# Kernel optimization log

Measured on AMD Instinct MI355X. Metric: run time of the kernel, lower is better.

Reference implementation:

```python
import jax, jax.numpy as jnp
import numpy as np

HIDDEN = 2048
HEADS = 16
HEAD_DIM = HIDDEN // HEADS
B, L = 4, 2048


def _rotate_half(x):
    x1, x2 = jnp.split(x, 2, axis=-1)
    return jnp.concatenate([-x2, x1], axis=-1)


def setup_inputs() -> dict:
    key = jax.random.key(0)
    k1, k2, k3 = jax.random.split(key, 3)
    x = jax.random.normal(k1, (B, L, HIDDEN), dtype=jnp.float32)
    # realistic rotary tables
    inv_freq = 1.0 / (10000.0 ** (jnp.arange(0, HEAD_DIM, 2, dtype=jnp.float32) / HEAD_DIM))
    t = jnp.arange(L, dtype=jnp.float32)
    freqs = jnp.outer(t, inv_freq)  # [L, HEAD_DIM/2]
    emb = jnp.concatenate([freqs, freqs], axis=-1)  # [L, HEAD_DIM]
    cos = jnp.cos(emb)
    sin = jnp.sin(emb)
    w_qkv = jax.random.normal(k2, (3 * HIDDEN, HIDDEN), dtype=jnp.float32) * (HIDDEN ** -0.5)
    w_out = jax.random.normal(k3, (HIDDEN, HIDDEN), dtype=jnp.float32) * (HIDDEN ** -0.5)
    return {"x": x, "cos": cos, "sin": sin, "w_qkv": w_qkv, "w_out": w_out}


def reference(x, cos, sin, w_qkv, w_out):
    b, l, d = x.shape
    qkv = jnp.einsum('bld,ed->ble', x, w_qkv)  # [B, L, 3D]
    q, k, v = jnp.split(qkv, 3, axis=-1)
    # [B, H, L, Dh]
    q = q.reshape(b, l, HEADS, HEAD_DIM).transpose(0, 2, 1, 3)
    k = k.reshape(b, l, HEADS, HEAD_DIM).transpose(0, 2, 1, 3)
    v = v.reshape(b, l, HEADS, HEAD_DIM).transpose(0, 2, 1, 3)
    cos_ = cos[None, None, :l, :]
    sin_ = sin[None, None, :l, :]
    q = q * cos_ + _rotate_half(q) * sin_
    k = k * cos_ + _rotate_half(k) * sin_
    scale = 1.0 / jnp.sqrt(jnp.asarray(HEAD_DIM, dtype=q.dtype))
    scores = jnp.einsum('bhqd,bhkd->bhqk', q, k) * scale
    attn = jax.nn.softmax(scores, axis=-1)
    out = jnp.einsum('bhqk,bhkd->bhqd', attn, v)  # [B, H, L, Dh]
    out = out.transpose(0, 2, 1, 3).reshape(b, l, d)
    return jnp.einsum('bld,ed->ble', out, w_out)
```

## Files before the change

### kernel.cpp

```cpp
#include <hip/hip_runtime.h>
#include <cstdint>
#include <cstddef>

typedef unsigned short u16;
typedef __attribute__((ext_vector_type(8))) short bf16x8;
typedef __attribute__((ext_vector_type(4))) float f32x4;

#define DEVFN static __device__ __forceinline__

DEVFN u16 f2bf(float f) {
  unsigned u = __float_as_uint(f);
  unsigned r = (u + 0x7FFFu + ((u >> 16) & 1u)) >> 16;
  return (u16)r;
}

DEVFN void gload16(const void* g, void* l) {
  __builtin_amdgcn_global_load_lds(
      (const __attribute__((address_space(1))) void*)g,
      (__attribute__((address_space(3))) void*)l, 16, 0, 0);
}

#define WAITVM(n) asm volatile("s_waitcnt vmcnt(" #n ")" ::: "memory")
#define BARRIER() do { asm volatile("" ::: "memory"); \
                       __builtin_amdgcn_s_barrier();   \
                       asm volatile("" ::: "memory"); } while (0)
#define FENCE_LDS() do { asm volatile("s_waitcnt lgkmcnt(0)" ::: "memory"); \
                         __builtin_amdgcn_sched_barrier(0); } while (0)

__global__ void prep(const float* __restrict__ x, const float* __restrict__ wqkv,
                     const float* __restrict__ wout, const float* __restrict__ cosp,
                     const float* __restrict__ sinp, u16* __restrict__ xb,
                     u16* __restrict__ wqkvb, u16* __restrict__ woutb,
                     float2* __restrict__ cs) {
  constexpr int X4 = 4194304;
  constexpr int W4 = 3145728;
  constexpr int O4 = 1048576;
  int i = blockIdx.x * blockDim.x + threadIdx.x;
  if (i < X4) {
    float4 v = ((const float4*)x)[i];
    unsigned long long w = (unsigned long long)f2bf(v.x)
        | ((unsigned long long)f2bf(v.y) << 16)
        | ((unsigned long long)f2bf(v.z) << 32)
        | ((unsigned long long)f2bf(v.w) << 48);
    *(unsigned long long*)(xb + (size_t)i * 4) = w;
  } else if (i < X4 + W4) {
    int j = i - X4;
    int base = j * 4;
    int e = base >> 11, col = base & 2047;
    int e2;
    if (e < 4096) {
      int part = e >> 11, loc = e & 2047;
      int h = loc >> 7, d = loc & 127;
      int d2 = (d < 64) ? 2 * d : 2 * (d - 64) + 1;
      e2 = part * 2048 + h * 128 + d2;
    } else {
      e2 = e;
    }
    float4 v = *(const float4*)&wqkv[(size_t)base];
    unsigned long long w = (unsigned long long)f2bf(v.x)
        | ((unsigned long long)f2bf(v.y) << 16)
        | ((unsigned long long)f2bf(v.z) << 32)
        | ((unsigned long long)f2bf(v.w) << 48);
    *(unsigned long long*)(wqkvb + (size_t)e2 * 2048 + col) = w;
  } else if (i < X4 + W4 + O4) {
    int j = i - X4 - W4;
    float4 v = ((const float4*)wout)[j];
    unsigned long long w = (unsigned long long)f2bf(v.x)
        | ((unsigned long long)f2bf(v.y) << 16)
        | ((unsigned long long)f2bf(v.z) << 32)
        | ((unsigned long long)f2bf(v.w) << 48);
    *(unsigned long long*)(woutb + (size_t)j * 4) = w;
  } else {
    int k = i - X4 - W4 - O4;
    int ld4 = k * 4;
#pragma unroll
    for (int u = 0; u < 4; u++) {
      int ld = ld4 + u;
      int l = ld >> 6, d = ld & 63;
      cs[ld] = make_float2(cosp[(size_t)l * 128 + d], sinp[(size_t)l * 128 + d]);
    }
  }
}

enum { M_F32OUT = 0, M_ROPE = 1, M_VT = 2 };

DEVFN bf16x8 rdfrag(const u16* buf, int row, int chunk) {
  return *(const bf16x8*)&buf[row * 64 + (((chunk ^ (row & 7)) & 7) << 3)];
}

template <int MODE, int Q>
DEVFN void phase_mfma(const u16* Ac, const u16* Bc, int wm, int wn, int quad, int l16,
                      bf16x8 (&bfr)[4][2], f32x4 (&acc)[8][4]) {
  if (Q == 0) {
#pragma unroll
    for (int j = 0; j < 4; j++)
#pragma unroll
      for (int kk = 0; kk < 2; kk++)
        bfr[j][kk] = rdfrag(Bc, wn * 64 + j * 16 + l16, kk * 4 + quad);
  }
  bf16x8 af[2][2];
#pragma unroll
  for (int i2 = 0; i2 < 2; i2++)
#pragma unroll
    for (int kk = 0; kk < 2; kk++)
      af[i2][kk] = rdfrag(Ac, wm * 128 + (Q * 2 + i2) * 16 + l16, kk * 4 + quad);
  __builtin_amdgcn_s_setprio(1);
#pragma unroll
  for (int kk = 0; kk < 2; kk++)
#pragma unroll
    for (int i2 = 0; i2 < 2; i2++)
#pragma unroll
      for (int j = 0; j < 4; j++) {
        if (MODE == M_VT)
          acc[Q * 2 + i2][j] = __builtin_amdgcn_mfma_f32_16x16x32_bf16(
              bfr[j][kk], af[i2][kk], acc[Q * 2 + i2][j], 0, 0, 0);
        else
          acc[Q * 2 + i2][j] = __builtin_amdgcn_mfma_f32_16x16x32_bf16(
              af[i2][kk], bfr[j][kk], acc[Q * 2 + i2][j], 0, 0, 0);
      }
  __builtin_amdgcn_s_setprio(0);
}

template <int MODE>
DEVFN void gemm256_core(const u16* __restrict__ A, const u16* __restrict__ Bt,
                        void* __restrict__ Cv, const float2* __restrict__ cs,
                        int N, int m0, int n0, u16* As, u16* Bs) {
  int tid = threadIdx.x;
  int wv = tid >> 6, lane = tid & 63, quad = lane >> 4, l16 = lane & 15;
  int wm = wv >> 2, wn = wv & 3;

  const u16* pB[2][2];
  const u16* pA[4];
#pragma unroll
  for (int h = 0; h < 2; h++)
#pragma unroll
    for (int o = 0; o < 2; o++) {
      int r = h * 128 + o * 64 + wv * 8 + (lane >> 3);
      int ck = (lane & 7) ^ (r & 7);
      pB[h][o] = Bt + (size_t)(n0 + r) * 2048 + ck * 8;
    }
#pragma unroll
  for (int q = 0; q < 4; q++) {
    int rb = (wv < 4) ? (q * 32 + wv * 8) : (128 + q * 32 + (wv - 4) * 8);
    int r = rb + (lane >> 3);
    int ck = (lane & 7) ^ (r & 7);
    pA[q] = A + (size_t)(m0 + r) * 2048 + ck * 8;
  }

#define STAGE_B(h, buf, kk) do {                                    \
    int rb0_ = (h) * 128 + wv * 8;                                  \
    gload16(pB[h][0] + (kk), &(buf)[rb0_ * 64]);                    \
    gload16(pB[h][1] + (kk), &(buf)[(rb0_ + 64) * 64]); } while (0)
#define STAGE_A(q, buf, kk) do {                                    \
    int rb_ = ((wv < 4) ? ((q) * 32 + wv * 8)                       \
                        : (128 + (q) * 32 + (wv - 4) * 8));         \
    gload16(pA[q] + (kk), &(buf)[rb_ * 64]); } while (0)

  f32x4 acc[8][4] = {};
  bf16x8 bfr[4][2];

  STAGE_B(0, Bs, 0);
  STAGE_B(1, Bs, 0);
  STAGE_A(0, As, 0);
  STAGE_A(1, As, 0);
  STAGE_A(2, As, 0);
  STAGE_A(3, As, 0);

  for (int t = 0; t < 31; t++) {
    const u16* Ac = As + (t & 1) * 16384;
    const u16* Bc = Bs + (t & 1) * 16384;
    u16* An = As + ((t + 1) & 1) * 16384;
    u16* Bn = Bs + ((t + 1) & 1) * 16384;
    int kn = (t + 1) * 64;
    STAGE_B(0, Bn, kn);
    WAITVM(5); BARRIER();
    phase_mfma<MODE, 0>(Ac, Bc, wm, wn, quad, l16, bfr, acc);
    STAGE_B(1, Bn, kn);
    WAITVM(6); BARRIER();
    phase_mfma<MODE, 1>(Ac, Bc, wm, wn, quad, l16, bfr, acc);
    STAGE_A(0, An, kn);
    STAGE_A(1, An, kn);
    WAITVM(7); BARRIER();
    phase_mfma<MODE, 2>(Ac, Bc, wm, wn, quad, l16, bfr, acc);
    STAGE_A(2, An, kn);
    STAGE_A(3, An, kn);
    WAITVM(8); BARRIER();
    phase_mfma<MODE, 3>(Ac, Bc, wm, wn, quad, l16, bfr, acc);
  }
  {
    const u16* Ac = As + 16384;
    const u16* Bc = Bs + 16384;
    WAITVM(3); BARRIER();
    phase_mfma<MODE, 0>(Ac, Bc, wm, wn, quad, l16, bfr, acc);
    WAITVM(2); BARRIER();
    phase_mfma<MODE, 1>(Ac, Bc, wm, wn, quad, l16, bfr, acc);
    WAITVM(1); BARRIER();
    phase_mfma<MODE, 2>(Ac, Bc, wm, wn, quad, l16, bfr, acc);
    WAITVM(0); BARRIER();
    phase_mfma<MODE, 3>(Ac, Bc, wm, wn, quad, l16, bfr, acc);
  }
#undef STAGE_B
#undef STAGE_A

  if (MODE == M_F32OUT) {
    float* C = (float*)Cv;
#pragma unroll
    for (int i = 0; i < 8; i++)
#pragma unroll
      for (int r = 0; r < 4; r++) {
        size_t row = (size_t)(m0 + wm * 128 + i * 16 + quad * 4 + r);
#pragma unroll
        for (int j = 0; j < 4; j++)
          C[row * N + (n0 + wn * 64 + j * 16 + l16)] = acc[i][j][r];
      }
  } else if (MODE == M_ROPE) {
    constexpr float QSCALE = 1.4426950408889634f * 0.08838834764831845f;
    const float scale = (n0 >> 11) ? 1.0f : QSCALE;
    u16* C = (u16*)Cv;
#pragma unroll
    for (int i = 0; i < 8; i++)
#pragma unroll
      for (int r = 0; r < 4; r++) {
        int row = m0 + wm * 128 + i * 16 + quad * 4 + r;
        int l = row & 2047;
#pragma unroll
        for (int j = 0; j < 4; j++) {
          int col = n0 + wn * 64 + j * 16 + l16;
          int dm = (col & 127) >> 1;
          float2 csv = cs[l * 64 + dm];
          float v = acc[i][j][r];
          float pv = __shfl_xor(v, 1);
          float sg = (l16 & 1) ? csv.y : -csv.y;
          C[(size_t)row * 4096 + col] = f2bf((v * csv.x + pv * sg) * scale);
        }
      }
  } else {
    u16* vt = (u16*)Cv;
#pragma unroll
    for (int j = 0; j < 4; j++)
#pragma unroll
      for (int r = 0; r < 4; r++) {
        int vch = n0 + wn * 64 + j * 16 + quad * 4 + r;
        int h = vch >> 7, d = vch & 127;
#pragma unroll
        for (int i = 0; i < 8; i++) {
          int token = m0 + wm * 128 + i * 16 + l16;
          int b = token >> 11, lloc = token & 2047;
          vt[((size_t)(b * 16 + h)) * 262144 + (size_t)d * 2048 + lloc] =
              f2bf(acc[i][j][r]);
        }
      }
  }
}

__global__ __launch_bounds__(512, 2) void gemm_qkv(const u16* __restrict__ xb,
                                                   const u16* __restrict__ wqkvb,
                                                   u16* __restrict__ qkvo,
                                                   u16* __restrict__ vto,
                                                   const float2* __restrict__ cs) {
  __shared__ u16 As[32768];
  __shared__ u16 Bs[32768];
  int id = blockIdx.x;
  int xcd = id & 7, sub = id >> 3;
  int bx = sub % 24, by = xcd * 4 + sub / 24;
  if (bx < 16)
    gemm256_core<M_ROPE>(xb, wqkvb, qkvo, cs, 0, by * 256, bx * 256, As, Bs);
  else
    gemm256_core<M_VT>(xb, wqkvb + (size_t)4096 * 2048, vto, nullptr, 0,
                       by * 256, (bx - 16) * 256, As, Bs);
}

__global__ __launch_bounds__(512, 2) void gemm_out_k(const u16* __restrict__ A,
                                                     const u16* __restrict__ Bt,
                                                     float* __restrict__ C) {
  __shared__ u16 As[32768];
  __shared__ u16 Bs[32768];
  int id = blockIdx.x;
  int xcd = id & 7, sub = id >> 3;
  int bx = sub % 8, by = xcd * 4 + sub / 8;
  gemm256_core<M_F32OUT>(A, Bt, C, nullptr, 2048, by * 256, bx * 256, As, Bs);
}

DEVFN int swz(int row, int chunk)   { return row * 128 + ((chunk ^ (row & 15)) << 3); }
DEVFN int swz32(int row, int chunk) { return row * 32  + (((chunk ^ (row & 3)) & 3) << 3); }

__global__ __launch_bounds__(256, 3) void attn_fused(const u16* __restrict__ qkv,
                                                     const u16* __restrict__ vt,
                                                     u16* __restrict__ out) {
  __shared__ u16 S[21504];
  u16* const Pb = S + 16384;
  int tid = threadIdx.x;
  int wv = tid >> 6, lane = tid & 63, quad = lane >> 4, l16 = lane & 15;
  int id = blockIdx.x;
  int xcd = id & 7, sub = id >> 3;
  int bh = ((sub >> 4) << 3) | xcd;
  int qt = sub & 15;
  int b = bh >> 4, hh = bh & 15;
  const u16* qptr = qkv + (size_t)b * 2048 * 4096 + hh * 128;
  const u16* kptr = qptr + 2048;
  const u16* vptr = vt + (size_t)bh * 262144;
  int q0 = qt * 128;

#pragma unroll
  for (int j = 0; j < 8; j++) {
    int rb = wv * 4 + j * 16;
    int r = rb + (lane >> 4);
    int ck = (lane & 15) ^ (r & 15);
    gload16(&qptr[(size_t)(q0 + r) * 4096 + ck * 8], &S[rb * 128]);
  }
  __syncthreads();
  bf16x8 qf[2][4];
#pragma unroll
  for (int hf = 0; hf < 2; hf++)
#pragma unroll
    for (int ks = 0; ks < 4; ks++)
      qf[hf][ks] = *(const bf16x8*)&S[swz(wv * 32 + hf * 16 + l16, ks * 4 + quad)];
  __syncthreads();

  f32x4 o[2][8] = {};
  float l[2][4] = {{0.f, 0.f, 0.f, 0.f}, {0.f, 0.f, 0.f, 0.f}};

#pragma unroll
  for (int j = 0; j < 2; j++) {
    int rbk = wv * 4 + j * 16;
    int rk = rbk + (lane >> 4);
    int ckk = (lane & 15) ^ (rk & 15);
    gload16(&kptr[(size_t)rk * 4096 + ckk * 8], &S[rbk * 128]);
    int rbv = wv * 16 + j * 64;
    int rv = rbv + (lane >> 2);
    int ckv = (lane & 3) ^ (rv & 3);
    gload16(&vptr[(size_t)rv * 2048 + ckv * 8], &S[8192 + rbv * 32]);
  }

  for (int kt = 0; kt < 64; kt++) {
    int cur = kt & 1;
    const u16* Kc = S + cur * 4096;
    const u16* Vc = S + 8192 + cur * 4096;
    __syncthreads();
    if (kt < 63) {
      int kk0 = (kt + 1) * 32;
      u16* kb = S + (cur ^ 1) * 4096;
      u16* vb = S + 8192 + (cur ^ 1) * 4096;
#pragma unroll
      for (int j = 0; j < 2; j++) {
        int rbk = wv * 4 + j * 16;
        int rk = rbk + (lane >> 4);
        int ckk = (lane & 15) ^ (rk & 15);
        gload16(&kptr[(size_t)(kk0 + rk) * 4096 + ckk * 8], &kb[rbk * 128]);
        int rbv = wv * 16 + j * 64;
        int rv = rbv + (lane >> 2);
        int ckv = (lane & 3) ^ (rv & 3);
        gload16(&vptr[(size_t)rv * 2048 + kk0 + ckv * 8], &vb[rbv * 32]);
      }
    }
    f32x4 s[2][2] = {};
#pragma unroll
    for (int ks = 0; ks < 4; ks++) {
#pragma unroll
      for (int nt = 0; nt < 2; nt++) {
        bf16x8 bfr = *(const bf16x8*)&Kc[swz(nt * 16 + l16, ks * 4 + quad)];
        s[0][nt] = __builtin_amdgcn_mfma_f32_16x16x32_bf16(qf[0][ks], bfr, s[0][nt], 0, 0, 0);
        s[1][nt] = __builtin_amdgcn_mfma_f32_16x16x32_bf16(qf[1][ks], bfr, s[1][nt], 0, 0, 0);
      }
    }
#pragma unroll
    for (int hf = 0; hf < 2; hf++)
#pragma unroll
      for (int nt = 0; nt < 2; nt++)
#pragma unroll
        for (int r = 0; r < 4; r++) {
          float p = exp2f(s[hf][nt][r]);
          l[hf][r] += p;
          int row = wv * 32 + hf * 16 + quad * 4 + r;
          int col = nt * 16 + l16;
          Pb[row * 40 + col] = f2bf(p);
        }
    FENCE_LDS();
    {
      bf16x8 pf0 = *(const bf16x8*)&Pb[(wv * 32 + l16) * 40 + quad * 8];
      bf16x8 pf1 = *(const bf16x8*)&Pb[(wv * 32 + 16 + l16) * 40 + quad * 8];
#pragma unroll
      for (int nt = 0; nt < 8; nt++) {
        bf16x8 vf = *(const bf16x8*)&Vc[swz32(nt * 16 + l16, quad)];
        o[0][nt] = __builtin_amdgcn_mfma_f32_16x16x32_bf16(pf0, vf, o[0][nt], 0, 0, 0);
        o[1][nt] = __builtin_amdgcn_mfma_f32_16x16x32_bf16(pf1, vf, o[1][nt], 0, 0, 0);
      }
    }
  }
#pragma unroll
  for (int hf = 0; hf < 2; hf++)
#pragma unroll
    for (int r = 0; r < 4; r++)
#pragma unroll
      for (int off = 1; off < 16; off <<= 1) l[hf][r] += __shfl_xor(l[hf][r], off, 16);
  u16* obase = out + ((size_t)b * 2048 + q0) * 2048 + hh * 128;
#pragma unroll
  for (int hf = 0; hf < 2; hf++)
#pragma unroll
    for (int r = 0; r < 4; r++) {
      float inv = 1.0f / l[hf][r];
      int row = wv * 32 + hf * 16 + quad * 4 + r;
#pragma unroll
      for (int nt = 0; nt < 8; nt++)
        obase[(size_t)row * 2048 + nt * 16 + l16] = f2bf(o[hf][nt][r] * inv);
    }
}

extern "C" void kernel_launch(void* const* d_in, const int* in_sizes, int n_in,
                              void* d_out, int out_size, void* d_ws, size_t ws_size,
                              hipStream_t stream) {
  const float* x    = (const float*)d_in[0];
  const float* cosp = (const float*)d_in[1];
  const float* sinp = (const float*)d_in[2];
  const float* wqkv = (const float*)d_in[3];
  const float* wout = (const float*)d_in[4];
  float* outp = (float*)d_out;

  u16* ws    = (u16*)d_ws;
  u16* xb    = ws;
  u16* wqkvb = xb + 16777216;
  u16* woutb = wqkvb + 12582912;
  u16* qkv   = woutb + 4194304;
  u16* vt    = qkv + 33554432;
  float2* cs = (float2*)(vt + 16777216);
  u16* attn  = xb;

  prep<<<32896, 256, 0, stream>>>(x, wqkv, wout, cosp, sinp, xb, wqkvb, woutb, cs);
  gemm_qkv<<<768, 512, 0, stream>>>(xb, wqkvb, qkv, vt, cs);
  attn_fused<<<1024, 256, 0, stream>>>(qkv, vt, attn);
  gemm_out_k<<<256, 512, 0, stream>>>(attn, woutb, outp);
}
```

Before: 616.9 us.

## Single-buffer GEMM LDS tiles with per-phase refill to fit two blocks per CU

Replaces the double-buffered A/B LDS tiles in both projection GEMMs with a single buffer, halving shared memory per block. Each slice of the next K tile is loaded into the same buffer only after the phase that last read it has drained its LDS reads and passed a barrier. The aim is to let two 512-thread blocks co-reside per CU, matching the launch bounds. In exchange there are extra barriers and LDS waits per K step and less prefetch lead time within a block, which relies on phase order lining up with what each phase reads.

```diff
diff --git a/kernel.cpp b/kernel.cpp
--- a/kernel.cpp
+++ b/kernel.cpp
@@ -24,6 +24,10 @@
 #define BARRIER() do { asm volatile("" ::: "memory"); \
                        __builtin_amdgcn_s_barrier();   \
                        asm volatile("" ::: "memory"); } while (0)
+#define PHASE_END() do { asm volatile("s_waitcnt lgkmcnt(0)" ::: "memory"); \
+                         __builtin_amdgcn_sched_barrier(0);                 \
+                         __builtin_amdgcn_s_barrier();                      \
+                         asm volatile("" ::: "memory"); } while (0)
 #define FENCE_LDS() do { asm volatile("s_waitcnt lgkmcnt(0)" ::: "memory"); \
                          __builtin_amdgcn_sched_barrier(0); } while (0)
 
@@ -147,57 +151,56 @@
     pA[q] = A + (size_t)(m0 + r) * 2048 + ck * 8;
   }
 
-#define STAGE_B(h, buf, kk) do {                                    \
+#define STAGE_B(h, kk) do {                                         \
     int rb0_ = (h) * 128 + wv * 8;                                  \
-    gload16(pB[h][0] + (kk), &(buf)[rb0_ * 64]);                    \
-    gload16(pB[h][1] + (kk), &(buf)[(rb0_ + 64) * 64]); } while (0)
-#define STAGE_A(q, buf, kk) do {                                    \
+    gload16(pB[h][0] + (kk), &Bs[rb0_ * 64]);                       \
+    gload16(pB[h][1] + (kk), &Bs[(rb0_ + 64) * 64]); } while (0)
+#define STAGE_A(q, kk) do {                                         \
     int rb_ = ((wv < 4) ? ((q) * 32 + wv * 8)                       \
                         : (128 + (q) * 32 + (wv - 4) * 8));         \
-    gload16(pA[q] + (kk), &(buf)[rb_ * 64]); } while (0)
+    gload16(pA[q] + (kk), &As[rb_ * 64]); } while (0)
 
   f32x4 acc[8][4] = {};
   bf16x8 bfr[4][2];
 
-  STAGE_B(0, Bs, 0);
-  STAGE_B(1, Bs, 0);
-  STAGE_A(0, As, 0);
-  STAGE_A(1, As, 0);
-  STAGE_A(2, As, 0);
-  STAGE_A(3, As, 0);
+  STAGE_B(0, 0);
+  STAGE_B(1, 0);
+  STAGE_A(0, 0);
+  STAGE_A(1, 0);
+  STAGE_A(2, 0);
+  STAGE_A(3, 0);
 
   for (int t = 0; t < 31; t++) {
-    const u16* Ac = As + (t & 1) * 16384;
-    const u16* Bc = Bs + (t & 1) * 16384;
-    u16* An = As + ((t + 1) & 1) * 16384;
-    u16* Bn = Bs + ((t + 1) & 1) * 16384;
     int kn = (t + 1) * 64;
-    STAGE_B(0, Bn, kn);
-    WAITVM(5); BARRIER();
-    phase_mfma<MODE, 0>(Ac, Bc, wm, wn, quad, l16, bfr, acc);
-    STAGE_B(1, Bn, kn);
-    WAITVM(6); BARRIER();
-    phase_mfma<MODE, 1>(Ac, Bc, wm, wn, quad, l16, bfr, acc);
-    STAGE_A(0, An, kn);
-    STAGE_A(1, An, kn);
+    WAITVM(3); BARRIER();
+    phase_mfma<MODE, 0>(As, Bs, wm, wn, quad, l16, bfr, acc);
+    PHASE_END();
+    STAGE_B(0, kn); STAGE_B(1, kn); STAGE_A(0, kn);
     WAITVM(7); BARRIER();
-    phase_mfma<MODE, 2>(Ac, Bc, wm, wn, quad, l16, bfr, acc);
-    STAGE_A(2, An, kn);
-    STAGE_A(3, An, kn);
-    WAITVM(8); BARRIER();
-    phase_mfma<MODE, 3>(Ac, Bc, wm, wn, quad, l16, bfr, acc);
+    phase_mfma<MODE, 1>(As, Bs, wm, wn, quad, l16, bfr, acc);
+    PHASE_END();
+    STAGE_A(1, kn);
+    WAITVM(7); BARRIER();
+    phase_mfma<MODE, 2>(As, Bs, wm, wn, quad, l16, bfr, acc);
+    PHASE_END();
+    STAGE_A(2, kn);
+    WAITVM(7); BARRIER();
+    phase_mfma<MODE, 3>(As, Bs, wm, wn, quad, l16, bfr, acc);
+    PHASE_END();
+    STAGE_A(3, kn);
   }
   {
-    const u16* Ac = As + 16384;
-    const u16* Bc = Bs + 16384;
     WAITVM(3); BARRIER();
-    phase_mfma<MODE, 0>(Ac, Bc, wm, wn, quad, l16, bfr, acc);
+    phase_mfma<MODE, 0>(As, Bs, wm, wn, quad, l16, bfr, acc);
+    PHASE_END();
     WAITVM(2); BARRIER();
-    phase_mfma<MODE, 1>(Ac, Bc, wm, wn, quad, l16, bfr, acc);
+    phase_mfma<MODE, 1>(As, Bs, wm, wn, quad, l16, bfr, acc);
+    PHASE_END();
     WAITVM(1); BARRIER();
-    phase_mfma<MODE, 2>(Ac, Bc, wm, wn, quad, l16, bfr, acc);
+    phase_mfma<MODE, 2>(As, Bs, wm, wn, quad, l16, bfr, acc);
+    PHASE_END();
     WAITVM(0); BARRIER();
-    phase_mfma<MODE, 3>(Ac, Bc, wm, wn, quad, l16, bfr, acc);
+    phase_mfma<MODE, 3>(As, Bs, wm, wn, quad, l16, bfr, acc);
   }
 #undef STAGE_B
 #undef STAGE_A
@@ -258,8 +261,8 @@
                                                    u16* __restrict__ qkvo,
                                                    u16* __restrict__ vto,
                                                    const float2* __restrict__ cs) {
-  __shared__ u16 As[32768];
-  __shared__ u16 Bs[32768];
+  __shared__ u16 As[16384];
+  __shared__ u16 Bs[16384];
   int id = blockIdx.x;
   int xcd = id & 7, sub = id >> 3;
   int bx = sub % 24, by = xcd * 4 + sub / 24;
@@ -273,8 +276,8 @@
 __global__ __launch_bounds__(512, 2) void gemm_out_k(const u16* __restrict__ A,
                                                      const u16* __restrict__ Bt,
                                                      float* __restrict__ C) {
-  __shared__ u16 As[32768];
-  __shared__ u16 Bs[32768];
+  __shared__ u16 As[16384];
+  __shared__ u16 Bs[16384];
   int id = blockIdx.x;
   int xcd = id & 7, sub = id >> 3;
   int bx = sub % 8, by = xcd * 4 + sub / 8;
```

After: 728.8 us. 1.18x slower.

## Merge four MFMA phases into two halves to halve per-tile barriers

Applied to the files above, without the earlier changes.

Restructures the GEMM main loop so each K-tile is processed in two MFMA halves instead of four quarters, cutting barriers and vmcnt waits per iteration from four to two. Each half now loads twice as many A fragments before issuing its MFMAs. This reduces synchronization overhead but coarsens the interleaving of global-to-LDS loads with compute, and raises register pressure from the larger fragment buffer.

```diff
diff --git a/kernel.cpp b/kernel.cpp
--- a/kernel.cpp
+++ b/kernel.cpp
@@ -88,36 +88,42 @@
   return *(const bf16x8*)&buf[row * 64 + (((chunk ^ (row & 7)) & 7) << 3)];
 }
 
-template <int MODE, int Q>
-DEVFN void phase_mfma(const u16* Ac, const u16* Bc, int wm, int wn, int quad, int l16,
-                      bf16x8 (&bfr)[4][2], f32x4 (&acc)[8][4]) {
-  if (Q == 0) {
+template <int MODE, int H>
+DEVFN void half_mfma(const u16* Ac, const u16* Bc, int wm, int wn, int quad, int l16,
+                     bf16x8 (&bfr)[4][2], f32x4 (&acc)[8][4]) {
+  if (H == 0) {
 #pragma unroll
     for (int j = 0; j < 4; j++)
 #pragma unroll
       for (int kk = 0; kk < 2; kk++)
         bfr[j][kk] = rdfrag(Bc, wn * 64 + j * 16 + l16, kk * 4 + quad);
   }
-  bf16x8 af[2][2];
-#pragma unroll
-  for (int i2 = 0; i2 < 2; i2++)
+  bf16x8 af[2][2][2];
+#pragma unroll
+  for (int qi = 0; qi < 2; qi++)
+#pragma unroll
+    for (int i2 = 0; i2 < 2; i2++)
+#pragma unroll
+      for (int kk = 0; kk < 2; kk++)
+        af[qi][i2][kk] =
+            rdfrag(Ac, wm * 128 + ((H * 2 + qi) * 2 + i2) * 16 + l16, kk * 4 + quad);
+  __builtin_amdgcn_s_setprio(1);
+#pragma unroll
+  for (int qi = 0; qi < 2; qi++)
 #pragma unroll
     for (int kk = 0; kk < 2; kk++)
-      af[i2][kk] = rdfrag(Ac, wm * 128 + (Q * 2 + i2) * 16 + l16, kk * 4 + quad);
-  __builtin_amdgcn_s_setprio(1);
-#pragma unroll
-  for (int kk = 0; kk < 2; kk++)
-#pragma unroll
-    for (int i2 = 0; i2 < 2; i2++)
-#pragma unroll
-      for (int j = 0; j < 4; j++) {
-        if (MODE == M_VT)
-          acc[Q * 2 + i2][j] = __builtin_amdgcn_mfma_f32_16x16x32_bf16(
-              bfr[j][kk], af[i2][kk], acc[Q * 2 + i2][j], 0, 0, 0);
-        else
-          acc[Q * 2 + i2][j] = __builtin_amdgcn_mfma_f32_16x16x32_bf16(
-              af[i2][kk], bfr[j][kk], acc[Q * 2 + i2][j], 0, 0, 0);
-      }
+#pragma unroll
+      for (int i2 = 0; i2 < 2; i2++)
+#pragma unroll
+        for (int j = 0; j < 4; j++) {
+          int row = (H * 2 + qi) * 2 + i2;
+          if (MODE == M_VT)
+            acc[row][j] = __builtin_amdgcn_mfma_f32_16x16x32_bf16(
+                bfr[j][kk], af[qi][i2][kk], acc[row][j], 0, 0, 0);
+          else
+            acc[row][j] = __builtin_amdgcn_mfma_f32_16x16x32_bf16(
+                af[qi][i2][kk], bfr[j][kk], acc[row][j], 0, 0, 0);
+        }
   __builtin_amdgcn_s_setprio(0);
 }
 
@@ -173,31 +179,23 @@
     u16* Bn = Bs + ((t + 1) & 1) * 16384;
     int kn = (t + 1) * 64;
     STAGE_B(0, Bn, kn);
-    WAITVM(5); BARRIER();
-    phase_mfma<MODE, 0>(Ac, Bc, wm, wn, quad, l16, bfr, acc);
     STAGE_B(1, Bn, kn);
     WAITVM(6); BARRIER();
-    phase_mfma<MODE, 1>(Ac, Bc, wm, wn, quad, l16, bfr, acc);
+    half_mfma<MODE, 0>(Ac, Bc, wm, wn, quad, l16, bfr, acc);
     STAGE_A(0, An, kn);
     STAGE_A(1, An, kn);
-    WAITVM(7); BARRIER();
-    phase_mfma<MODE, 2>(Ac, Bc, wm, wn, quad, l16, bfr, acc);
     STAGE_A(2, An, kn);
     STAGE_A(3, An, kn);
     WAITVM(8); BARRIER();
-    phase_mfma<MODE, 3>(Ac, Bc, wm, wn, quad, l16, bfr, acc);
+    half_mfma<MODE, 1>(Ac, Bc, wm, wn, quad, l16, bfr, acc);
   }
   {
     const u16* Ac = As + 16384;
     const u16* Bc = Bs + 16384;
-    WAITVM(3); BARRIER();
-    phase_mfma<MODE, 0>(Ac, Bc, wm, wn, quad, l16, bfr, acc);
     WAITVM(2); BARRIER();
-    phase_mfma<MODE, 1>(Ac, Bc, wm, wn, quad, l16, bfr, acc);
-    WAITVM(1); BARRIER();
-    phase_mfma<MODE, 2>(Ac, Bc, wm, wn, quad, l16, bfr, acc);
+    half_mfma<MODE, 0>(Ac, Bc, wm, wn, quad, l16, bfr, acc);
     WAITVM(0); BARRIER();
-    phase_mfma<MODE, 3>(Ac, Bc, wm, wn, quad, l16, bfr, acc);
+    half_mfma<MODE, 1>(Ac, Bc, wm, wn, quad, l16, bfr, acc);
   }
 #undef STAGE_B
 #undef STAGE_A
```

Measured after the change: 588.3 us. -4.6%, faster.

## Split GEMM phases into LDS fragment reads and MFMA bursts with extra barriers

Applied to the files above, without the earlier changes.

Splits each GEMM phase into a fragment-read step and an MFMA-only step, separated by barriers, in the style of a ping-pong schedule. LDS fragment reads are issued before the next global-to-LDS stage and its waitcnt, so different waves can overlap LDS reads with matrix math. It doubles the number of barriers per K step and retunes the vmcnt thresholds, which adds sync overhead and risks read/write hazards on the double buffer if the counts are wrong.

```diff
diff --git a/kernel.cpp b/kernel.cpp
--- a/kernel.cpp
+++ b/kernel.cpp
@@ -88,9 +88,9 @@
   return *(const bf16x8*)&buf[row * 64 + (((chunk ^ (row & 7)) & 7) << 3)];
 }
 
-template <int MODE, int Q>
-DEVFN void phase_mfma(const u16* Ac, const u16* Bc, int wm, int wn, int quad, int l16,
-                      bf16x8 (&bfr)[4][2], f32x4 (&acc)[8][4]) {
+template <int Q>
+DEVFN void read_frags(const u16* Ac, const u16* Bc, int wm, int wn, int quad, int l16,
+                      bf16x8 (&bfr)[4][2], bf16x8 (&af)[2][2]) {
   if (Q == 0) {
 #pragma unroll
     for (int j = 0; j < 4; j++)
@@ -98,12 +98,15 @@
       for (int kk = 0; kk < 2; kk++)
         bfr[j][kk] = rdfrag(Bc, wn * 64 + j * 16 + l16, kk * 4 + quad);
   }
-  bf16x8 af[2][2];
 #pragma unroll
   for (int i2 = 0; i2 < 2; i2++)
 #pragma unroll
     for (int kk = 0; kk < 2; kk++)
       af[i2][kk] = rdfrag(Ac, wm * 128 + (Q * 2 + i2) * 16 + l16, kk * 4 + quad);
+}
+
+template <int MODE, int Q>
+DEVFN void mfma_only(bf16x8 (&bfr)[4][2], bf16x8 (&af)[2][2], f32x4 (&acc)[8][4]) {
   __builtin_amdgcn_s_setprio(1);
 #pragma unroll
   for (int kk = 0; kk < 2; kk++)
@@ -158,6 +161,7 @@
 
   f32x4 acc[8][4] = {};
   bf16x8 bfr[4][2];
+  bf16x8 af[2][2];
 
   STAGE_B(0, Bs, 0);
   STAGE_B(1, Bs, 0);
@@ -165,6 +169,7 @@
   STAGE_A(1, As, 0);
   STAGE_A(2, As, 0);
   STAGE_A(3, As, 0);
+  WAITVM(3); BARRIER();
 
   for (int t = 0; t < 31; t++) {
     const u16* Ac = As + (t & 1) * 16384;
@@ -172,32 +177,47 @@
     u16* An = As + ((t + 1) & 1) * 16384;
     u16* Bn = Bs + ((t + 1) & 1) * 16384;
     int kn = (t + 1) * 64;
+    read_frags<0>(Ac, Bc, wm, wn, quad, l16, bfr, af);
     STAGE_B(0, Bn, kn);
+    WAITVM(4); BARRIER();
+    mfma_only<MODE, 0>(bfr, af, acc);
+    BARRIER();
+    read_frags<1>(Ac, Bc, wm, wn, quad, l16, bfr, af);
+    STAGE_B(1, Bn, kn);
     WAITVM(5); BARRIER();
-    phase_mfma<MODE, 0>(Ac, Bc, wm, wn, quad, l16, bfr, acc);
-    STAGE_B(1, Bn, kn);
-    WAITVM(6); BARRIER();
-    phase_mfma<MODE, 1>(Ac, Bc, wm, wn, quad, l16, bfr, acc);
+    mfma_only<MODE, 1>(bfr, af, acc);
+    BARRIER();
+    read_frags<2>(Ac, Bc, wm, wn, quad, l16, bfr, af);
     STAGE_A(0, An, kn);
     STAGE_A(1, An, kn);
-    WAITVM(7); BARRIER();
-    phase_mfma<MODE, 2>(Ac, Bc, wm, wn, quad, l16, bfr, acc);
+    WAITVM(6); BARRIER();
+    mfma_only<MODE, 2>(bfr, af, acc);
+    BARRIER();
+    read_frags<3>(Ac, Bc, wm, wn, quad, l16, bfr, af);
     STAGE_A(2, An, kn);
     STAGE_A(3, An, kn);
-    WAITVM(8); BARRIER();
-    phase_mfma<MODE, 3>(Ac, Bc, wm, wn, quad, l16, bfr, acc);
+    WAITVM(3); BARRIER();
+    mfma_only<MODE, 3>(bfr, af, acc);
+    BARRIER();
   }
   {
     const u16* Ac = As + 16384;
     const u16* Bc = Bs + 16384;
-    WAITVM(3); BARRIER();
-    phase_mfma<MODE, 0>(Ac, Bc, wm, wn, quad, l16, bfr, acc);
+    read_frags<0>(Ac, Bc, wm, wn, quad, l16, bfr, af);
     WAITVM(2); BARRIER();
-    phase_mfma<MODE, 1>(Ac, Bc, wm, wn, quad, l16, bfr, acc);
+    mfma_only<MODE, 0>(bfr, af, acc);
+    BARRIER();
+    read_frags<1>(Ac, Bc, wm, wn, quad, l16, bfr, af);
     WAITVM(1); BARRIER();
-    phase_mfma<MODE, 2>(Ac, Bc, wm, wn, quad, l16, bfr, acc);
+    mfma_only<MODE, 1>(bfr, af, acc);
+    BARRIER();
+    read_frags<2>(Ac, Bc, wm, wn, quad, l16, bfr, af);
     WAITVM(0); BARRIER();
-    phase_mfma<MODE, 3>(Ac, Bc, wm, wn, quad, l16, bfr, acc);
+    mfma_only<MODE, 2>(bfr, af, acc);
+    BARRIER();
+    read_frags<3>(Ac, Bc, wm, wn, quad, l16, bfr, af);
+    BARRIER();
+    mfma_only<MODE, 3>(bfr, af, acc);
   }
 #undef STAGE_B
 #undef STAGE_A
```

New measurement: 602.3 us. 2.4% less time.
